# Performance work log

Measured on AMD Instinct MI355X. Metric: run time of the kernel, lower is better.

The kernel has to match this reference:

```python
import jax, jax.numpy as jnp
import numpy as np

B, L, D, H = 4, 1024, 256, 8
TEMP = float(np.sqrt(D))
EPS_SM = 1e-6
EPS_LN = 1e-5


def setup_inputs() -> dict:
    key = jax.random.key(0)
    ks = jax.random.split(key, 8)
    std = float(np.sqrt(2.0 / (D * 2)))
    return {
        "q": jax.random.normal(ks[0], (B, L, D), jnp.float32),
        "mask": jax.random.randint(ks[1], (B, L, L), 0, 2, jnp.int32),
        "k": jax.random.normal(ks[2], (B, L, D), jnp.float32),
        "v": jax.random.normal(ks[3], (B, L, D), jnp.float32),
        "w_qs": jax.random.normal(ks[4], (H * D, D), jnp.float32) * std,
        "w_ks": jax.random.normal(ks[5], (H * D, D), jnp.float32) * std,
        "w_vs": jax.random.normal(ks[6], (H * D, D), jnp.float32) * std,
        "fc_w": jax.random.normal(ks[7], (D, H * D), jnp.float32) * float(np.sqrt(2.0 / (D + H * D))),
        "fc_b": jnp.zeros((D,), jnp.float32),
        "ln_g": jnp.ones((D,), jnp.float32),
        "ln_b": jnp.zeros((D,), jnp.float32),
    }


def masked_softmax(x, m):
    # repo's layers.masked_softmax: clamp, mask-mul, stable exp, mask-mul, normalize
    x = jnp.clip(x, -15.0, 15.0) * m
    e = jnp.exp(x - jnp.max(x, axis=-1, keepdims=True)) * m
    return e / (jnp.sum(e, axis=-1, keepdims=True) + EPS_SM)


def reference(q, mask, k, v, w_qs, w_ks, w_vs, fc_w, fc_b, ln_g, ln_b):
    residual = q
    m = mask.astype(q.dtype)[:, None, :, :]          # [B,1,Lq,Lk]
    # projections to per-head full-dim: [B,L,H,D]
    qh = (q @ w_qs.T).reshape(B, L, H, D)
    kh = (k @ w_ks.T).reshape(B, L, H, D)
    vh = (v @ w_vs.T).reshape(B, L, H, D)
    scores = jnp.einsum("bqhd,bkhd->bhqk", qh, kh) / TEMP   # [B,H,Lq,Lk]
    attn = masked_softmax(scores, m)
    out = jnp.einsum("bhqk,bkhd->bqhd", attn, vh).reshape(B, L, H * D)
    out = out @ fc_w.T + fc_b                         # [B,L,D]
    out = out + residual
    mu = jnp.mean(out, axis=-1, keepdims=True)
    var = jnp.var(out, axis=-1, keepdims=True)
    out = (out - mu) / jnp.sqrt(var + EPS_LN) * ln_g + ln_b
    # match torch attn layout: [H*B, Lq, Lk] (head-major)
    attn_hb = jnp.transpose(attn, (1, 0, 2, 3)).reshape(H * B, L, L)
    return out, attn_hb
```

## Files before the change

kernel.cpp:

```cpp
#include <hip/hip_runtime.h>
#include <cstdint>
#include <math.h>

#define Bsz 4
#define Lsz 1024
#define Dsz 256
#define Hsz 8
#define HD  2048
#define NROWS (Bsz*Lsz)
#define INV_TEMP 0.0625f

typedef __attribute__((ext_vector_type(8))) short bf16x8;
typedef __attribute__((ext_vector_type(4))) float f32x4;

__device__ inline unsigned short f2bf(float f) {
    union { float f; unsigned u; } x; x.f = f;
    unsigned r = x.u + 0x7fffu + ((x.u >> 16) & 1u);
    return (unsigned short)(r >> 16);
}
__device__ inline float bf2f(unsigned short u) {
    union { unsigned u; float f; } x; x.u = (unsigned)u << 16; return x.f;
}

#define GBL(p) ((const __attribute__((address_space(1))) unsigned int*)(p))
#define LDS(p) ((__attribute__((address_space(3))) unsigned int*)(p))

template <int TMv, int TNv, typename OutT, int EPI, int MINW>
__global__ __launch_bounds__(256, MINW) void gemm_bt(
    const unsigned short* __restrict__ A, const unsigned short* __restrict__ Bm,
    OutT* __restrict__ C,
    int K, int lda, int ldb, int ldc, int inner,
    long long sA1, long long sA2, long long sB1, long long sB2,
    long long sC1, long long sC2, float alpha,
    const unsigned short* __restrict__ maskb, long long sM2,
    const float* __restrict__ invs, long long sI1, long long sI2,
    float* __restrict__ aux)
{
    constexpr int WMv = TMv / 2, WNv = TNv / 2;
    constexpr int IT = TMv / 32, JT = TNv / 32;
    constexpr int APASS = TMv / 32, NPASS = (TMv + TNv) / 32;
    constexpr int TILE = (TMv + TNv) * 64;
    static_assert(NPASS == 6, "vmcnt literals below assume NPASS==6");

    const int z  = blockIdx.z;
    const int i1 = z / inner;
    const int i2 = z % inner;
    A  += (size_t)i1 * sA1 + (size_t)i2 * sA2;
    Bm += (size_t)i1 * sB1 + (size_t)i2 * sB2;
    C  += (size_t)i1 * sC1 + (size_t)i2 * sC2;
    if (EPI == 1) { maskb += (size_t)i2 * sM2; aux += (size_t)z * Lsz; }
    if (EPI == 2) { invs  += (size_t)i1 * sI1 + (size_t)i2 * sI2; aux += (size_t)z * Lsz * Lsz; }

    __shared__ unsigned short S[2 * TILE];
    __shared__ float inv_lds[EPI == 2 ? TMv : 1];

    const int t    = threadIdx.x;
    const int lane = t & 63;
    const int w    = t >> 6;
    const int wm   = w & 1;
    const int wn   = w >> 1;
    const int m0   = blockIdx.x * TMv;
    const int n0   = blockIdx.y * TNv;

    const int rA = t >> 3;
    const int ch = ((t & 7) ^ (rA & 7)) * 8;
    const unsigned short* gA = A  + (size_t)(m0 + rA) * lda + ch;
    const unsigned short* gB = Bm + (size_t)(n0 + rA) * ldb + ch;

    const int fr = lane & 15;
    const int q  = lane >> 4;

    f32x4 acc[IT][JT];
#pragma unroll
    for (int i = 0; i < IT; ++i)
#pragma unroll
        for (int j = 0; j < JT; ++j) acc[i][j] = (f32x4){0.f, 0.f, 0.f, 0.f};

    auto stage = [&](unsigned short* Sb, int k0) {
#pragma unroll
        for (int p = 0; p < NPASS; ++p) {
            const unsigned short* src = (p < APASS)
                ? (gA + (size_t)p * 32 * lda + k0)
                : (gB + (size_t)(p - APASS) * 32 * ldb + k0);
            __builtin_amdgcn_global_load_lds(GBL(src), LDS(Sb + p * 2048 + t * 8), 16, 0, 0);
        }
    };
    auto kstep = [&](const unsigned short* As) {
        const unsigned short* Bs = As + TMv * 64;
#pragma unroll
        for (int ks = 0; ks < 2; ++ks) {
            const int slot = ((ks * 4 + q) ^ (fr & 7)) * 8;
            bf16x8 a[IT], b[JT];
#pragma unroll
            for (int i = 0; i < IT; ++i)
                a[i] = *(const bf16x8*)(As + (wm * WMv + i * 16 + fr) * 64 + slot);
#pragma unroll
            for (int j = 0; j < JT; ++j)
                b[j] = *(const bf16x8*)(Bs + (wn * WNv + j * 16 + fr) * 64 + slot);
#pragma unroll
            for (int i = 0; i < IT; ++i)
#pragma unroll
                for (int j = 0; j < JT; ++j)
                    acc[i][j] = __builtin_amdgcn_mfma_f32_16x16x32_bf16(a[i], b[j], acc[i][j], 0, 0, 0);
        }
    };

    const int nk = K >> 6;
    const bool y1 = (blockIdx.y == 1);

    stage(S, 0);
    if constexpr (EPI == 2) {
        if (t < TMv) inv_lds[t] = 1.0f / (invs[m0 + t] + 1e-6f);
        __syncthreads();
    }

    for (int kt = 0; kt < nk; ++kt) {
        if (kt + 1 < nk) stage(S + ((kt + 1) & 1) * TILE, (kt + 1) << 6);

        if constexpr (EPI == 2) {
            const bool pstore = (kt >= 1) && (((kt - 1) >= (nk >> 1)) == y1);
            if (kt + 1 < nk) {
                if (pstore) asm volatile("s_waitcnt vmcnt(10)" ::: "memory");
                else        asm volatile("s_waitcnt vmcnt(6)"  ::: "memory");
            } else {
                if (pstore) asm volatile("s_waitcnt vmcnt(4)"  ::: "memory");
                else        asm volatile("s_waitcnt vmcnt(0)"  ::: "memory");
            }
        } else {
            if (kt + 1 < nk) asm volatile("s_waitcnt vmcnt(6)" ::: "memory");
            else             asm volatile("s_waitcnt vmcnt(0)" ::: "memory");
        }
        __builtin_amdgcn_s_barrier();

        kstep(S + (kt & 1) * TILE);

        if constexpr (EPI == 2) {
            if ((kt >= (nk >> 1)) == y1) {
                const unsigned short* As = S + (kt & 1) * TILE;
                const int chunk = lane & 7;
                const int rsub  = lane >> 3;
#pragma unroll
                for (int pass = 0; pass < TMv / 32; ++pass) {
                    const int row = w * (TMv / 4) + pass * 8 + rsub;
                    const uint4 u = *(const uint4*)(As + row * 64 + ((chunk ^ (row & 7)) * 8));
                    const float iv = inv_lds[row];
                    float4 lo, hi;
                    lo.x = bf2f((unsigned short)(u.x & 0xffff)) * iv; lo.y = bf2f((unsigned short)(u.x >> 16)) * iv;
                    lo.z = bf2f((unsigned short)(u.y & 0xffff)) * iv; lo.w = bf2f((unsigned short)(u.y >> 16)) * iv;
                    hi.x = bf2f((unsigned short)(u.z & 0xffff)) * iv; hi.y = bf2f((unsigned short)(u.z >> 16)) * iv;
                    hi.z = bf2f((unsigned short)(u.w & 0xffff)) * iv; hi.w = bf2f((unsigned short)(u.w >> 16)) * iv;
                    float* op = aux + (size_t)(m0 + row) * Lsz + (kt << 6) + chunk * 8;
                    *(float4*)op = lo;
                    *(float4*)(op + 4) = hi;
                }
            }
        }

        asm volatile("s_waitcnt lgkmcnt(0)" ::: "memory");
        __builtin_amdgcn_s_barrier();
    }

#pragma unroll
    for (int i = 0; i < IT; ++i) {
#pragma unroll
        for (int r = 0; r < 4; ++r) {
            const int row = m0 + wm * WMv + i * 16 + q * 4 + r;
            float rsum = 0.f;
#pragma unroll
            for (int j = 0; j < JT; ++j) {
                const int col = n0 + wn * WNv + j * 16 + fr;
                float vv = acc[i][j][r] * alpha;
                if (EPI == 0) {
                    if constexpr (sizeof(OutT) == 4)
                        C[(size_t)row * ldc + col] = (OutT)vv;
                    else
                        ((unsigned short*)C)[(size_t)row * ldc + col] = f2bf(vv);
                } else if (EPI == 1) {
                    const float m = bf2f(maskb[(size_t)row * Lsz + col]);
                    vv = fminf(fmaxf(vv, -15.f), 15.f) * m;
                    vv = __expf(vv) * m;
                    const unsigned short us = f2bf(vv);
                    ((unsigned short*)C)[(size_t)row * ldc + col] = us;
                    rsum += bf2f(us);
                } else {
                    vv *= inv_lds[row - m0];
                    ((unsigned short*)C)[(size_t)row * ldc + col] = f2bf(vv);
                }
            }
            if constexpr (EPI == 1) {
#pragma unroll
                for (int o = 1; o <= 8; o <<= 1) rsum += __shfl_xor(rsum, o, 64);
                if (fr == 0) atomicAdd(&aux[row], rsum);
            }
        }
    }
}

__global__ __launch_bounds__(256) void cast_all(
    const float* __restrict__ q, const float* __restrict__ k, const float* __restrict__ v,
    const float* __restrict__ wq, const float* __restrict__ wk, const float* __restrict__ wv,
    const float* __restrict__ fw, const int* __restrict__ mask,
    unsigned short* __restrict__ qb, unsigned short* __restrict__ kb, unsigned short* __restrict__ vb,
    unsigned short* __restrict__ wqb, unsigned short* __restrict__ wkb, unsigned short* __restrict__ wvb,
    unsigned short* __restrict__ fwb, unsigned short* __restrict__ mb,
    float* __restrict__ rs)
{
    const int gid = blockIdx.x * 256 + threadIdx.x;
    const int NQ = 262144;
    const int NW = 131072;
    const int NF = 3 * NQ + 4 * NW;
    const int NM = 1048576;
    if (gid >= NF) {
        const int off = gid - NF;
        if (off >= NM) {
            const int ri = off - NM;
            if (ri < 8192) ((float4*)rs)[ri] = (float4){0.f, 0.f, 0.f, 0.f};
            return;
        }
        const int4 mi = ((const int4*)mask)[off];
        ushort4 o;
        o.x = mi.x ? 0x3F80 : 0;
        o.y = mi.y ? 0x3F80 : 0;
        o.z = mi.z ? 0x3F80 : 0;
        o.w = mi.w ? 0x3F80 : 0;
        ((ushort4*)mb)[off] = o;
        return;
    }
    const float* src; unsigned short* dst; int off;
    if      (gid < NQ)            { src = q;  dst = qb;  off = gid; }
    else if (gid < 2 * NQ)        { src = k;  dst = kb;  off = gid - NQ; }
    else if (gid < 3 * NQ)        { src = v;  dst = vb;  off = gid - 2 * NQ; }
    else if (gid < 3 * NQ + NW)   { src = wq; dst = wqb; off = gid - 3 * NQ; }
    else if (gid < 3 * NQ + 2*NW) { src = wk; dst = wkb; off = gid - 3 * NQ - NW; }
    else if (gid < 3 * NQ + 3*NW) { src = wv; dst = wvb; off = gid - 3 * NQ - 2 * NW; }
    else                          { src = fw; dst = fwb; off = gid - 3 * NQ - 3 * NW; }
    float4 f = ((const float4*)src)[off];
    ushort4 o;
    o.x = f2bf(f.x); o.y = f2bf(f.y); o.z = f2bf(f.z); o.w = f2bf(f.w);
    ((ushort4*)dst)[off] = o;
}

__global__ __launch_bounds__(256) void ln_kernel(const float* __restrict__ gout,
                                                 const float* __restrict__ qin,
                                                 const float* __restrict__ fc_b,
                                                 const float* __restrict__ ln_g,
                                                 const float* __restrict__ ln_b,
                                                 float* __restrict__ out)
{
    const int row = blockIdx.x;
    const int t = threadIdx.x;
    const size_t idx = (size_t)row * Dsz + t;
    const size_t P = (size_t)NROWS * Dsz;
    const float val = gout[idx] + gout[idx + P] + gout[idx + 2 * P] + gout[idx + 3 * P]
                    + fc_b[t] + qin[idx];

    __shared__ float red[4];
    float s = val;
#pragma unroll
    for (int o = 32; o > 0; o >>= 1) s += __shfl_down(s, o, 64);
    const int lane = t & 63, w = t >> 6;
    if (lane == 0) red[w] = s;
    __syncthreads();
    const float mu = (red[0] + red[1] + red[2] + red[3]) * (1.0f / Dsz);
    __syncthreads();

    float d = val - mu;
    float s2 = d * d;
#pragma unroll
    for (int o = 32; o > 0; o >>= 1) s2 += __shfl_down(s2, o, 64);
    if (lane == 0) red[w] = s2;
    __syncthreads();
    const float var = (red[0] + red[1] + red[2] + red[3]) * (1.0f / Dsz);

    out[idx] = d * rsqrtf(var + 1e-5f) * ln_g[t] + ln_b[t];
}

extern "C" void kernel_launch(void* const* d_in, const int* in_sizes, int n_in,
                              void* d_out, int out_size, void* d_ws, size_t ws_size,
                              hipStream_t stream)
{
    const float* q    = (const float*)d_in[0];
    const int*   mask = (const int*)d_in[1];
    const float* k    = (const float*)d_in[2];
    const float* v    = (const float*)d_in[3];
    const float* w_qs = (const float*)d_in[4];
    const float* w_ks = (const float*)d_in[5];
    const float* w_vs = (const float*)d_in[6];
    const float* fc_w = (const float*)d_in[7];
    const float* fc_b = (const float*)d_in[8];
    const float* ln_g = (const float*)d_in[9];
    const float* ln_b = (const float*)d_in[10];

    float* out  = (float*)d_out;
    float* attn = (float*)d_out + (size_t)NROWS * Dsz;

    unsigned short* wsu = (unsigned short*)d_ws;
    unsigned short* qh     = wsu;
    unsigned short* kh     = qh + (size_t)NROWS * HD;
    unsigned short* q_bf   = kh + (size_t)NROWS * HD;
    unsigned short* k_bf   = q_bf + (size_t)NROWS * Dsz;
    unsigned short* v_bf   = k_bf + (size_t)NROWS * Dsz;
    unsigned short* wq_bf  = v_bf + (size_t)NROWS * Dsz;
    unsigned short* wk_bf  = wq_bf + (size_t)HD * Dsz;
    unsigned short* wv_bf  = wk_bf + (size_t)HD * Dsz;
    unsigned short* vt     = wv_bf + (size_t)HD * Dsz;
    unsigned short* attn_e = vt + (size_t)Bsz * HD * Lsz;
    unsigned short* attnv  = attn_e + (size_t)32 * Lsz * Lsz;
    unsigned short* fcw_bf = attnv + (size_t)NROWS * HD;
    float*          rowsum = (float*)(fcw_bf + (size_t)Dsz * HD);
    float*          fcout  = rowsum + 32768;
    unsigned short* maskb  = (unsigned short*)(fcout + (size_t)4 * NROWS * Dsz);

    dim3 blk(256);

    cast_all<<<dim3(9248), blk, 0, stream>>>(q, k, v, w_qs, w_ks, w_vs, fc_w, mask,
                                             q_bf, k_bf, v_bf, wq_bf, wk_bf, wv_bf, fcw_bf, maskb,
                                             rowsum);

    {
        dim3 grid(NROWS / 64, HD / 128, 2);
        gemm_bt<64, 128, unsigned short, 0, 3><<<grid, blk, 0, stream>>>(q_bf, wq_bf, qh,
            Dsz, Dsz, Dsz, HD, 2,
            0, (long long)NROWS * Dsz, 0, (long long)HD * Dsz, 0, (long long)NROWS * HD,
            1.0f, nullptr, 0, nullptr, 0, 0, nullptr);
    }

    {
        dim3 grid(HD / 64, Lsz / 128, Bsz);
        gemm_bt<64, 128, unsigned short, 0, 3><<<grid, blk, 0, stream>>>(wv_bf, v_bf, vt,
            Dsz, Dsz, Dsz, Lsz, 1,
            0, 0, (long long)Lsz * Dsz, 0, (long long)HD * Lsz, 0,
            1.0f, nullptr, 0, nullptr, 0, 0, nullptr);
    }

    {
        dim3 grid(Lsz / 64, Lsz / 128, Hsz * Bsz);
        gemm_bt<64, 128, unsigned short, 1, 3><<<grid, blk, 0, stream>>>(qh, kh, attn_e,
            Dsz, HD, HD, Lsz, Bsz,
            Dsz, (long long)Lsz * HD, Dsz, (long long)Lsz * HD,
            (long long)Bsz * Lsz * Lsz, (long long)Lsz * Lsz,
            INV_TEMP, maskb, (long long)Lsz * Lsz, nullptr, 0, 0, rowsum);
    }

    {
        dim3 grid(Lsz / 64, Dsz / 128, Hsz * Bsz);
        gemm_bt<64, 128, unsigned short, 2, 3><<<grid, blk, 0, stream>>>(attn_e, vt, attnv,
            Lsz, Lsz, Lsz, HD, Bsz,
            (long long)Bsz * Lsz * Lsz, (long long)Lsz * Lsz,
            (long long)Dsz * Lsz, (long long)HD * Lsz,
            Dsz, (long long)Lsz * HD,
            1.0f, nullptr, 0, rowsum, (long long)Bsz * Lsz, (long long)Lsz, attn);
    }

    {
        dim3 grid(NROWS / 64, Dsz / 128, 4);
        gemm_bt<64, 128, float, 0, 3><<<grid, blk, 0, stream>>>(attnv, fcw_bf, fcout,
            512, HD, HD, Dsz, 4,
            0, 512, 0, 512, 0, (long long)NROWS * Dsz,
            1.0f, nullptr, 0, nullptr, 0, 0, nullptr);
    }

    ln_kernel<<<dim3(NROWS), blk, 0, stream>>>(fcout, q, fc_b, ln_g, ln_b, out);
}
```

Baseline: 335.6 us.

## Fuse V projection into QK projection launch and widen attn@V tile

```diff
diff --git a/kernel.cpp b/kernel.cpp
--- a/kernel.cpp
+++ b/kernel.cpp
@@ -25,7 +25,16 @@
 #define GBL(p) ((const __attribute__((address_space(1))) unsigned int*)(p))
 #define LDS(p) ((__attribute__((address_space(3))) unsigned int*)(p))
 
-template <int TMv, int TNv, typename OutT, int EPI, int MINW>
+template<int N> __device__ __forceinline__ void vmw() {
+    if constexpr (N == 0)       asm volatile("s_waitcnt vmcnt(0)"  ::: "memory");
+    else if constexpr (N == 4)  asm volatile("s_waitcnt vmcnt(4)"  ::: "memory");
+    else if constexpr (N == 6)  asm volatile("s_waitcnt vmcnt(6)"  ::: "memory");
+    else if constexpr (N == 10) asm volatile("s_waitcnt vmcnt(10)" ::: "memory");
+    else if constexpr (N == 14) asm volatile("s_waitcnt vmcnt(14)" ::: "memory");
+    else static_assert(N == 0, "unsupported vmcnt literal");
+}
+
+template <int TMv, int TNv, typename OutT, int EPI, int MINW, bool FUSE>
 __global__ __launch_bounds__(256, MINW) void gemm_bt(
     const unsigned short* __restrict__ A, const unsigned short* __restrict__ Bm,
     OutT* __restrict__ C,
@@ -34,33 +43,53 @@
     long long sC1, long long sC2, float alpha,
     const unsigned short* __restrict__ maskb, long long sM2,
     const float* __restrict__ invs, long long sI1, long long sI2,
-    float* __restrict__ aux)
+    float* __restrict__ aux,
+    const unsigned short* __restrict__ A2, const unsigned short* __restrict__ B2,
+    unsigned short* __restrict__ C2)
 {
     constexpr int WMv = TMv / 2, WNv = TNv / 2;
     constexpr int IT = TMv / 32, JT = TNv / 32;
     constexpr int APASS = TMv / 32, NPASS = (TMv + TNv) / 32;
     constexpr int TILE = (TMv + TNv) * 64;
-    static_assert(NPASS == 6, "vmcnt literals below assume NPASS==6");
+    static_assert(NPASS == 6 || NPASS == 10, "vmcnt literals assume NPASS in {6,10}");
 
     const int z  = blockIdx.z;
-    const int i1 = z / inner;
-    const int i2 = z % inner;
-    A  += (size_t)i1 * sA1 + (size_t)i2 * sA2;
-    Bm += (size_t)i1 * sB1 + (size_t)i2 * sB2;
-    C  += (size_t)i1 * sC1 + (size_t)i2 * sC2;
-    if (EPI == 1) { maskb += (size_t)i2 * sM2; aux += (size_t)z * Lsz; }
-    if (EPI == 2) { invs  += (size_t)i1 * sI1 + (size_t)i2 * sI2; aux += (size_t)z * Lsz * Lsz; }
+    int mx = blockIdx.x, my = blockIdx.y;
+
+    if constexpr (FUSE) {
+        if (z >= 2) {
+            const int idx = my * 64 + mx;
+            if (idx >= 256) return;
+            mx = idx & 31; my = idx >> 5;
+            const int b = z - 2;
+            A   = A2;
+            Bm  = B2 + (size_t)b * ((size_t)Lsz * Dsz);
+            C   = (OutT*)(C2 + (size_t)b * ((size_t)HD * Lsz));
+            ldc = Lsz;
+        } else {
+            A  += (size_t)z * sA2;
+            Bm += (size_t)z * sB2;
+            C  += (size_t)z * sC2;
+        }
+    } else {
+        const int i1 = z / inner;
+        const int i2 = z % inner;
+        A  += (size_t)i1 * sA1 + (size_t)i2 * sA2;
+        Bm += (size_t)i1 * sB1 + (size_t)i2 * sB2;
+        C  += (size_t)i1 * sC1 + (size_t)i2 * sC2;
+        if (EPI == 1) { maskb += (size_t)i2 * sM2; aux += (size_t)z * Lsz; }
+        if (EPI == 2) { invs  += (size_t)i1 * sI1 + (size_t)i2 * sI2; aux += (size_t)z * Lsz * Lsz; }
+    }
 
     __shared__ unsigned short S[2 * TILE];
-    __shared__ float inv_lds[EPI == 2 ? TMv : 1];
 
     const int t    = threadIdx.x;
     const int lane = t & 63;
     const int w    = t >> 6;
     const int wm   = w & 1;
     const int wn   = w >> 1;
-    const int m0   = blockIdx.x * TMv;
-    const int n0   = blockIdx.y * TNv;
+    const int m0   = mx * TMv;
+    const int n0   = my * TNv;
 
     const int rA = t >> 3;
     const int ch = ((t & 7) ^ (rA & 7)) * 8;
@@ -106,58 +135,61 @@
     };
 
     const int nk = K >> 6;
-    const bool y1 = (blockIdx.y == 1);
+
+    float ainv[EPI == 2 ? (TMv / 32) : 1];
+    if constexpr (EPI == 2) {
+        const int rsub = lane >> 3;
+#pragma unroll
+        for (int pass = 0; pass < TMv / 32; ++pass)
+            ainv[pass] = 1.0f / (invs[m0 + w * (TMv / 4) + pass * 8 + rsub] + 1e-6f);
+    }
 
     stage(S, 0);
-    if constexpr (EPI == 2) {
-        if (t < TMv) inv_lds[t] = 1.0f / (invs[m0 + t] + 1e-6f);
-        __syncthreads();
-    }
 
     for (int kt = 0; kt < nk; ++kt) {
         if (kt + 1 < nk) stage(S + ((kt + 1) & 1) * TILE, (kt + 1) << 6);
 
         if constexpr (EPI == 2) {
-            const bool pstore = (kt >= 1) && (((kt - 1) >= (nk >> 1)) == y1);
-            if (kt + 1 < nk) {
-                if (pstore) asm volatile("s_waitcnt vmcnt(10)" ::: "memory");
-                else        asm volatile("s_waitcnt vmcnt(6)"  ::: "memory");
-            } else {
-                if (pstore) asm volatile("s_waitcnt vmcnt(4)"  ::: "memory");
-                else        asm volatile("s_waitcnt vmcnt(0)"  ::: "memory");
-            }
+            if (kt + 1 < nk) { if (kt >= 1) vmw<NPASS + 4>(); else vmw<NPASS>(); }
+            else             { if (kt >= 1) vmw<4>();         else vmw<0>(); }
         } else {
-            if (kt + 1 < nk) asm volatile("s_waitcnt vmcnt(6)" ::: "memory");
-            else             asm volatile("s_waitcnt vmcnt(0)" ::: "memory");
+            if (kt + 1 < nk) vmw<NPASS>(); else vmw<0>();
         }
         __builtin_amdgcn_s_barrier();
 
         kstep(S + (kt & 1) * TILE);
 
         if constexpr (EPI == 2) {
-            if ((kt >= (nk >> 1)) == y1) {
-                const unsigned short* As = S + (kt & 1) * TILE;
-                const int chunk = lane & 7;
-                const int rsub  = lane >> 3;
-#pragma unroll
-                for (int pass = 0; pass < TMv / 32; ++pass) {
-                    const int row = w * (TMv / 4) + pass * 8 + rsub;
-                    const uint4 u = *(const uint4*)(As + row * 64 + ((chunk ^ (row & 7)) * 8));
-                    const float iv = inv_lds[row];
-                    float4 lo, hi;
-                    lo.x = bf2f((unsigned short)(u.x & 0xffff)) * iv; lo.y = bf2f((unsigned short)(u.x >> 16)) * iv;
-                    lo.z = bf2f((unsigned short)(u.y & 0xffff)) * iv; lo.w = bf2f((unsigned short)(u.y >> 16)) * iv;
-                    hi.x = bf2f((unsigned short)(u.z & 0xffff)) * iv; hi.y = bf2f((unsigned short)(u.z >> 16)) * iv;
-                    hi.z = bf2f((unsigned short)(u.w & 0xffff)) * iv; hi.w = bf2f((unsigned short)(u.w >> 16)) * iv;
-                    float* op = aux + (size_t)(m0 + row) * Lsz + (kt << 6) + chunk * 8;
-                    *(float4*)op = lo;
-                    *(float4*)(op + 4) = hi;
-                }
+            const unsigned short* As = S + (kt & 1) * TILE;
+            const int chunk = lane & 7;
+            const int rsub  = lane >> 3;
+#pragma unroll
+            for (int pass = 0; pass < TMv / 32; ++pass) {
+                const int row = w * (TMv / 4) + pass * 8 + rsub;
+                const uint4 u = *(const uint4*)(As + row * 64 + ((chunk ^ (row & 7)) * 8));
+                const float iv = ainv[pass];
+                float4 lo, hi;
+                lo.x = bf2f((unsigned short)(u.x & 0xffff)) * iv; lo.y = bf2f((unsigned short)(u.x >> 16)) * iv;
+                lo.z = bf2f((unsigned short)(u.y & 0xffff)) * iv; lo.w = bf2f((unsigned short)(u.y >> 16)) * iv;
+                hi.x = bf2f((unsigned short)(u.z & 0xffff)) * iv; hi.y = bf2f((unsigned short)(u.z >> 16)) * iv;
+                hi.z = bf2f((unsigned short)(u.w & 0xffff)) * iv; hi.w = bf2f((unsigned short)(u.w >> 16)) * iv;
+                float* op = aux + (size_t)(m0 + row) * Lsz + (kt << 6) + chunk * 8;
+                *(float4*)op = lo;
+                *(float4*)(op + 4) = hi;
             }
         }
 
         asm volatile("s_waitcnt lgkmcnt(0)" ::: "memory");
         __builtin_amdgcn_s_barrier();
+    }
+
+    float einv[EPI == 2 ? IT : 1][EPI == 2 ? 4 : 1];
+    if constexpr (EPI == 2) {
+#pragma unroll
+        for (int i = 0; i < IT; ++i)
+#pragma unroll
+            for (int r = 0; r < 4; ++r)
+                einv[i][r] = 1.0f / (invs[m0 + wm * WMv + i * 16 + q * 4 + r] + 1e-6f);
     }
 
 #pragma unroll
@@ -183,7 +215,7 @@
                     ((unsigned short*)C)[(size_t)row * ldc + col] = us;
                     rsum += bf2f(us);
                 } else {
-                    vv *= inv_lds[row - m0];
+                    vv *= einv[i][r];
                     ((unsigned short*)C)[(size_t)row * ldc + col] = f2bf(vv);
                 }
             }
@@ -318,46 +350,42 @@
                                              rowsum);
 
     {
-        dim3 grid(NROWS / 64, HD / 128, 2);
-        gemm_bt<64, 128, unsigned short, 0, 3><<<grid, blk, 0, stream>>>(q_bf, wq_bf, qh,
+        dim3 grid(NROWS / 64, HD / 128, 6);
+        gemm_bt<64, 128, unsigned short, 0, 3, true><<<grid, blk, 0, stream>>>(q_bf, wq_bf, qh,
             Dsz, Dsz, Dsz, HD, 2,
             0, (long long)NROWS * Dsz, 0, (long long)HD * Dsz, 0, (long long)NROWS * HD,
-            1.0f, nullptr, 0, nullptr, 0, 0, nullptr);
-    }
-
-    {
-        dim3 grid(HD / 64, Lsz / 128, Bsz);
-        gemm_bt<64, 128, unsigned short, 0, 3><<<grid, blk, 0, stream>>>(wv_bf, v_bf, vt,
-            Dsz, Dsz, Dsz, Lsz, 1,
-            0, 0, (long long)Lsz * Dsz, 0, (long long)HD * Lsz, 0,
-            1.0f, nullptr, 0, nullptr, 0, 0, nullptr);
+            1.0f, nullptr, 0, nullptr, 0, 0, nullptr,
+            wv_bf, v_bf, vt);
     }
 
     {
         dim3 grid(Lsz / 64, Lsz / 128, Hsz * Bsz);
-        gemm_bt<64, 128, unsigned short, 1, 3><<<grid, blk, 0, stream>>>(qh, kh, attn_e,
+        gemm_bt<64, 128, unsigned short, 1, 3, false><<<grid, blk, 0, stream>>>(qh, kh, attn_e,
             Dsz, HD, HD, Lsz, Bsz,
             Dsz, (long long)Lsz * HD, Dsz, (long long)Lsz * HD,
             (long long)Bsz * Lsz * Lsz, (long long)Lsz * Lsz,
-            INV_TEMP, maskb, (long long)Lsz * Lsz, nullptr, 0, 0, rowsum);
+            INV_TEMP, maskb, (long long)Lsz * Lsz, nullptr, 0, 0, rowsum,
+            nullptr, nullptr, nullptr);
     }
 
     {
-        dim3 grid(Lsz / 64, Dsz / 128, Hsz * Bsz);
-        gemm_bt<64, 128, unsigned short, 2, 3><<<grid, blk, 0, stream>>>(attn_e, vt, attnv,
+        dim3 grid(Lsz / 64, 1, Hsz * Bsz);
+        gemm_bt<64, 256, unsigned short, 2, 2, false><<<grid, blk, 0, stream>>>(attn_e, vt, attnv,
             Lsz, Lsz, Lsz, HD, Bsz,
             (long long)Bsz * Lsz * Lsz, (long long)Lsz * Lsz,
             (long long)Dsz * Lsz, (long long)HD * Lsz,
             Dsz, (long long)Lsz * HD,
-            1.0f, nullptr, 0, rowsum, (long long)Bsz * Lsz, (long long)Lsz, attn);
+            1.0f, nullptr, 0, rowsum, (long long)Bsz * Lsz, (long long)Lsz, attn,
+            nullptr, nullptr, nullptr);
     }
 
     {
         dim3 grid(NROWS / 64, Dsz / 128, 4);
-        gemm_bt<64, 128, float, 0, 3><<<grid, blk, 0, stream>>>(attnv, fcw_bf, fcout,
+        gemm_bt<64, 128, float, 0, 3, false><<<grid, blk, 0, stream>>>(attnv, fcw_bf, fcout,
             512, HD, HD, Dsz, 4,
             0, 512, 0, 512, 0, (long long)NROWS * Dsz,
-            1.0f, nullptr, 0, nullptr, 0, 0, nullptr);
+            1.0f, nullptr, 0, nullptr, 0, 0, nullptr,
+            nullptr, nullptr, nullptr);
     }
 
     ln_kernel<<<dim3(NROWS), blk, 0, stream>>>(fcout, q, fc_b, ln_g, ln_b, out);
```

Measured after the change: 331.2 us. Within noise of the previous version (-1.3%).
